# Performance work log

Hardware: AMD Instinct MI355X
Metric: run time of the kernel (lower is better)

Reference implementation:

```python
import jax, jax.numpy as jnp
import numpy as np

N_EMBD = 1024
N_HEADS = 16
HEAD_SIZE = N_EMBD // N_HEADS
B, T = 1, 4096
LN_EPS = 1e-5


def setup_inputs() -> dict:
    key = jax.random.key(0)
    ks = jax.random.split(key, 12)
    s = lambda fan_in: 1.0 / np.sqrt(fan_in)
    return {
        "x": jax.random.normal(ks[0], (B, T, N_EMBD), dtype=jnp.float32),
        # per-head Q/K/V projections (no bias), stacked over heads: [H, C, hd]
        "Wq": jax.random.normal(ks[1], (N_HEADS, N_EMBD, HEAD_SIZE), dtype=jnp.float32) * s(N_EMBD),
        "Wk": jax.random.normal(ks[2], (N_HEADS, N_EMBD, HEAD_SIZE), dtype=jnp.float32) * s(N_EMBD),
        "Wv": jax.random.normal(ks[3], (N_HEADS, N_EMBD, HEAD_SIZE), dtype=jnp.float32) * s(N_EMBD),
        # output projection (with bias)
        "Wp": jax.random.normal(ks[4], (N_EMBD, N_EMBD), dtype=jnp.float32) * s(N_EMBD),
        "bp": jnp.zeros((N_EMBD,), dtype=jnp.float32),
        # FFN: Linear(C, 4C) -> ReLU -> Linear(4C, C)
        "W1": jax.random.normal(ks[5], (N_EMBD, 4 * N_EMBD), dtype=jnp.float32) * s(N_EMBD),
        "b1": jnp.zeros((4 * N_EMBD,), dtype=jnp.float32),
        "W2": jax.random.normal(ks[6], (4 * N_EMBD, N_EMBD), dtype=jnp.float32) * s(4 * N_EMBD),
        "b2": jnp.zeros((N_EMBD,), dtype=jnp.float32),
        # LayerNorms
        "g1": jnp.ones((N_EMBD,), dtype=jnp.float32),
        "be1": jnp.zeros((N_EMBD,), dtype=jnp.float32),
        "g2": jnp.ones((N_EMBD,), dtype=jnp.float32),
        "be2": jnp.zeros((N_EMBD,), dtype=jnp.float32),
    }


def _layernorm(x, gamma, beta):
    mu = jnp.mean(x, axis=-1, keepdims=True)
    var = jnp.mean(jnp.square(x - mu), axis=-1, keepdims=True)
    return (x - mu) * jax.lax.rsqrt(var + LN_EPS) * gamma + beta


def _block(x, Wq, Wk, Wv, Wp, bp, W1, b1, W2, b2, g1, be1, g2, be2):
    Bn, Tn, C = x.shape
    h = _layernorm(x, g1, be1)
    # per-head projections: [B, H, T, hd]
    q = jnp.einsum("btc,hcd->bhtd", h, Wq)
    k = jnp.einsum("btc,hcd->bhtd", h, Wk)
    v = jnp.einsum("btc,hcd->bhtd", h, Wv)
    # NOTE: original scales by C**-0.5 where C = n_embd (not head_size)
    scores = jnp.einsum("bhtd,bhsd->bhts", q, k) * (C ** -0.5)
    causal = jnp.tril(jnp.ones((Tn, Tn), dtype=bool))
    scores = jnp.where(causal, scores, -jnp.inf)
    w = jax.nn.softmax(scores, axis=-1)
    attn = jnp.einsum("bhts,bhsd->bhtd", w, v)
    # concat heads: [B, T, H*hd] = [B, T, C]
    attn = attn.transpose(0, 2, 1, 3).reshape(Bn, Tn, C)
    x = x + attn @ Wp + bp
    h2 = _layernorm(x, g2, be2)
    ff = jax.nn.relu(h2 @ W1 + b1) @ W2 + b2
    return x + ff


def reference(x, Wq, Wk, Wv, Wp, bp, W1, b1, W2, b2, g1, be1, g2, be2):
    return _block(x, Wq, Wk, Wv, Wp, bp, W1, b1, W2, b2, g1, be1, g2, be2)
```

## Files before the change

kernel.cpp:

```cpp
#include <hip/hip_runtime.h>
#include <cstdint>

typedef __attribute__((ext_vector_type(8))) short bf16x8;
typedef __attribute__((ext_vector_type(4))) float f32x4;
typedef __attribute__((ext_vector_type(16))) float f32x16;
typedef __attribute__((ext_vector_type(4))) unsigned int u32x4;

__device__ __forceinline__ short f2b(float f) {
  unsigned u = __builtin_bit_cast(unsigned, f);
  unsigned r = (u + 0x7fffu + ((u >> 16) & 1u)) >> 16;
  return (short)(unsigned short)r;
}
__device__ __forceinline__ float b2f(short s) {
  unsigned u = ((unsigned)(unsigned short)s) << 16;
  return __builtin_bit_cast(float, u);
}

__device__ __forceinline__ void gload16(void* lds_dst, const void* gsrc) {
  __builtin_amdgcn_global_load_lds(
      (const __attribute__((address_space(1))) void*)gsrc,
      (__attribute__((address_space(3))) void*)lds_dst, 16, 0, 0);
}

__device__ __forceinline__ unsigned cvtpk(float a, float b) {
  unsigned r;
  asm("v_cvt_pk_bf16_f32 %0, %1, %2" : "=v"(r) : "v"(a), "v"(b));
  return r;
}
__device__ __forceinline__ unsigned shflx32(unsigned v) {
  return (unsigned)__shfl_xor((int)v, 32);
}
__device__ __forceinline__ float exp2x(float x) {
  float r;
  asm("v_exp_f32 %0, %1" : "=v"(r) : "v"(x));
  return r;
}

__device__ __forceinline__ void plswap(unsigned &a, unsigned &b) {
#if __has_builtin(__builtin_amdgcn_permlane32_swap)
  auto r = __builtin_amdgcn_permlane32_swap((int)a, (int)b, false, false);
  a = (unsigned)r[0];
  b = (unsigned)r[1];
#else
  const bool lo = ((threadIdx.x & 63) < 32);
  unsigned ax = shflx32(a), bx = shflx32(b);
  unsigned na = lo ? a : bx;
  unsigned nb = lo ? ax : b;
  a = na; b = nb;
#endif
}

__global__ __launch_bounds__(256)
void prep_all(const float* __restrict__ Wq, const float* __restrict__ Wk,
              const float* __restrict__ Wv, const float* __restrict__ Wp,
              const float* __restrict__ W1, const float* __restrict__ W2,
              const float* __restrict__ x, const float* __restrict__ g1,
              const float* __restrict__ be1,
              short* __restrict__ WqkvT, short* __restrict__ WpT,
              short* __restrict__ W1T, short* __restrict__ W2T,
              short* __restrict__ hbuf)
{
  const int id = blockIdx.x;
  if (id < 12288) {
    __shared__ float tl[32][33];
    const int tx = threadIdx.x & 31;
    const int ty = threadIdx.x >> 5;
    if (id < 3072) {
      const int which = id >> 10;
      const int rem = id & 1023;
      const int head = rem >> 6;
      const int tile = rem & 63;
      const int tc = tile >> 1, td = tile & 1;
      const float* src = (which == 0 ? Wq : which == 1 ? Wk : Wv) + (long)head * 65536;
#pragma unroll
      for (int i2 = 0; i2 < 4; ++i2) {
        int i = ty + i2 * 8;
        tl[i][tx] = src[(long)(tc * 32 + i) * 64 + td * 32 + tx];
      }
      __syncthreads();
      const long base = (long)which * 1024 + head * 64 + td * 32;
#pragma unroll
      for (int i2 = 0; i2 < 4; ++i2) {
        int i = ty + i2 * 8;
        WqkvT[(base + i) * 1024 + tc * 32 + tx] = f2b(tl[tx][i]);
      }
    } else {
      const float* src;
      short* dst;
      int rows, cols, bx, by;
      if (id < 4096) {
        src = Wp; dst = WpT; rows = 1024; cols = 1024;
        const int k = id - 3072; bx = k & 31; by = k >> 5;
      } else if (id < 8192) {
        src = W1; dst = W1T; rows = 1024; cols = 4096;
        const int k = id - 4096; bx = k & 127; by = k >> 7;
      } else {
        src = W2; dst = W2T; rows = 4096; cols = 1024;
        const int k = id - 8192; bx = k & 31; by = k >> 5;
      }
#pragma unroll
      for (int i2 = 0; i2 < 4; ++i2) {
        int i = ty + i2 * 8;
        tl[i][tx] = src[(long)(by * 32 + i) * cols + bx * 32 + tx];
      }
      __syncthreads();
#pragma unroll
      for (int i2 = 0; i2 < 4; ++i2) {
        int i = ty + i2 * 8;
        dst[(long)(bx * 32 + i) * rows + by * 32 + tx] = f2b(tl[tx][i]);
      }
    }
  } else {
    const int row = id - 12288;
    const int t = threadIdx.x;
    const float4 v = ((const float4*)(x + (long)row * 1024))[t];
    float s = v.x + v.y + v.z + v.w;
    float ss = v.x * v.x + v.y * v.y + v.z * v.z + v.w * v.w;
#pragma unroll
    for (int off = 1; off < 64; off <<= 1) {
      s += __shfl_xor(s, off);
      ss += __shfl_xor(ss, off);
    }
    __shared__ float red[8];
    const int wave = t >> 6, lane = t & 63;
    if (lane == 0) { red[wave] = s; red[4 + wave] = ss; }
    __syncthreads();
    s = red[0] + red[1] + red[2] + red[3];
    ss = red[4] + red[5] + red[6] + red[7];
    const float mu = s * (1.f / 1024.f);
    const float rstd = rsqrtf(ss * (1.f / 1024.f) - mu * mu + 1e-5f);
    const float4 gv = ((const float4*)g1)[t];
    const float4 bv = ((const float4*)be1)[t];
    short4 ov;
    ov.x = f2b((v.x - mu) * rstd * gv.x + bv.x);
    ov.y = f2b((v.y - mu) * rstd * gv.y + bv.y);
    ov.z = f2b((v.z - mu) * rstd * gv.z + bv.z);
    ov.w = f2b((v.w - mu) * rstd * gv.w + bv.w);
    *(short4*)(hbuf + (long)row * 1024 + t * 4) = ov;
  }
}

__global__ void vtrans(const short* __restrict__ qkv, short* __restrict__ Vt)
{
  __shared__ short tl[32][33];
  const int t0 = blockIdx.x * 32;
  const int c0 = blockIdx.y * 32;
  const int head = c0 >> 6, d0 = c0 & 63;
  const int tx = threadIdx.x;
#pragma unroll
  for (int i2 = 0; i2 < 4; ++i2) {
    int i = threadIdx.y + i2 * 8;
    tl[i][tx] = qkv[(long)(t0 + i) * 3072 + 2048 + c0 + tx];
  }
  __syncthreads();
#pragma unroll
  for (int i2 = 0; i2 < 4; ++i2) {
    int i = threadIdx.y + i2 * 8;
    Vt[(long)head * 262144 + (long)(d0 + i) * 4096 + t0 + tx] = tl[tx][i];
  }
}

__global__ __launch_bounds__(256)
void layernorm_bf16(const float* __restrict__ x, const float* __restrict__ g,
                    const float* __restrict__ be, short* __restrict__ outp)
{
  const int row = blockIdx.x;
  const int t = threadIdx.x;
  const float4 v = ((const float4*)(x + (long)row * 1024))[t];
  float s = v.x + v.y + v.z + v.w;
  float ss = v.x * v.x + v.y * v.y + v.z * v.z + v.w * v.w;
#pragma unroll
  for (int off = 1; off < 64; off <<= 1) {
    s += __shfl_xor(s, off);
    ss += __shfl_xor(ss, off);
  }
  __shared__ float red[8];
  const int wave = t >> 6, lane = t & 63;
  if (lane == 0) { red[wave] = s; red[4 + wave] = ss; }
  __syncthreads();
  s = red[0] + red[1] + red[2] + red[3];
  ss = red[4] + red[5] + red[6] + red[7];
  const float mu = s * (1.f / 1024.f);
  const float rstd = rsqrtf(ss * (1.f / 1024.f) - mu * mu + 1e-5f);
  const float4 gv = ((const float4*)g)[t];
  const float4 bv = ((const float4*)be)[t];
  short4 ov;
  ov.x = f2b((v.x - mu) * rstd * gv.x + bv.x);
  ov.y = f2b((v.y - mu) * rstd * gv.y + bv.y);
  ov.z = f2b((v.z - mu) * rstd * gv.z + bv.z);
  ov.w = f2b((v.w - mu) * rstd * gv.w + bv.w);
  *(short4*)(outp + (long)row * 1024 + t * 4) = ov;
}

template<int EPI>
__global__ __launch_bounds__(512, 2)
void gemm128(const short* __restrict__ A, const short* __restrict__ Bt,
             int N, int K, int NT,
             short* __restrict__ Cb, float* __restrict__ Cf,
             const float* __restrict__ bias, const float* __restrict__ resid)
{
  __shared__ __align__(16) short As[2 * 8192];
  __shared__ __align__(16) short Bs[2 * 8192];
  const int tid = threadIdx.x;
  const int lane = tid & 63;
  const int wave = tid >> 6;
  const int wm = wave >> 2;
  const int wn = wave & 3;
  const int l15 = lane & 15, lg = lane >> 4;

  const int nwg = gridDim.x * gridDim.y;
  const int lin = blockIdx.y * gridDim.x + blockIdx.x;
  const int swz = (lin & 7) * (nwg >> 3) + (lin >> 3);
  const long m0 = (long)(swz / gridDim.x) * 128;
  const long n0 = (long)(swz % gridDim.x) * 128;

  const int rloc = lane >> 3;
  const int csrc = (lane & 7) ^ rloc;
  const short* Ag = A + (m0 + wave * 8 + rloc) * K + csrc * 8;
  const short* Bg = Bt + (n0 + wave * 8 + rloc) * K + csrc * 8;
  const int wbase = wave * 512;

  f32x4 acc[4][2] = {};

#define STAGE128(buf, kt)                                                     \
  do {                                                                        \
    gload16(As + (buf) * 8192 + wbase, Ag + (kt));                            \
    gload16(As + (buf) * 8192 + 4096 + wbase, Ag + (long)64 * K + (kt));      \
    gload16(Bs + (buf) * 8192 + wbase, Bg + (kt));                            \
    gload16(Bs + (buf) * 8192 + 4096 + wbase, Bg + (long)64 * K + (kt));      \
  } while (0)

  STAGE128(0, 0);
  STAGE128(1, 64);
  asm volatile("s_waitcnt vmcnt(4)" ::: "memory");
  __builtin_amdgcn_sched_barrier(0);
  __builtin_amdgcn_s_barrier();
  __builtin_amdgcn_sched_barrier(0);

  const int cA = l15 & 7;
  for (int t = 0; t < NT; ++t) {
    const char* Ab = (const char*)(As + (t & 1) * 8192);
    const char* Bb = (const char*)(Bs + (t & 1) * 8192);
#pragma unroll
    for (int kk = 0; kk < 2; ++kk) {
      bf16x8 af[4], bk[2];
#pragma unroll
      for (int mi = 0; mi < 4; ++mi)
        af[mi] = *(const bf16x8*)(Ab + (wm * 64 + mi * 16 + l15) * 128 + 16 * ((kk * 4 + lg) ^ cA));
#pragma unroll
      for (int ni = 0; ni < 2; ++ni)
        bk[ni] = *(const bf16x8*)(Bb + (wn * 32 + ni * 16 + l15) * 128 + 16 * ((kk * 4 + lg) ^ cA));
      __builtin_amdgcn_s_setprio(1);
#pragma unroll
      for (int mi = 0; mi < 4; ++mi)
#pragma unroll
        for (int ni = 0; ni < 2; ++ni)
          acc[mi][ni] = __builtin_amdgcn_mfma_f32_16x16x32_bf16(af[mi], bk[ni], acc[mi][ni], 0, 0, 0);
      __builtin_amdgcn_s_setprio(0);
    }
    if (t == NT - 1) break;
    __builtin_amdgcn_s_barrier();
    __builtin_amdgcn_sched_barrier(0);
    if (t + 2 < NT) {
      STAGE128(t & 1, (long)(t + 2) * 64);
      asm volatile("s_waitcnt vmcnt(4)" ::: "memory");
    } else {
      asm volatile("s_waitcnt vmcnt(0)" ::: "memory");
    }
    __builtin_amdgcn_sched_barrier(0);
    __builtin_amdgcn_s_barrier();
    __builtin_amdgcn_sched_barrier(0);
  }
#undef STAGE128

#pragma unroll
  for (int mi = 0; mi < 4; ++mi) {
#pragma unroll
    for (int ni = 0; ni < 2; ++ni) {
      const long col = n0 + wn * 32 + ni * 16 + l15;
#pragma unroll
      for (int r = 0; r < 4; ++r) {
        const long row = m0 + wm * 64 + mi * 16 + lg * 4 + r;
        const long idx = row * N + col;
        float v = acc[mi][ni][r];
        if (EPI == 0) {
          Cb[idx] = f2b(v);
        } else {
          Cf[idx] = v + bias[col] + resid[idx];
        }
      }
    }
  }
}

__device__ __forceinline__ void stage256(short* AsB, short* BsB,
                                         const short* Ag, const short* Bg,
                                         long kt, int K, int ldsoff)
{
#pragma unroll
  for (int p = 0; p < 4; ++p)
    gload16(AsB + p * 4096 + ldsoff, Ag + (long)p * 64 * K + kt);
#pragma unroll
  for (int p = 0; p < 4; ++p)
    gload16(BsB + p * 4096 + ldsoff, Bg + (long)p * 64 * K + kt);
}

template<int EPI>
__global__ __launch_bounds__(512, 2)
void gemm256(const short* __restrict__ A, const short* __restrict__ Bt,
             int N, int K, int NT,
             short* __restrict__ Cb, const float* __restrict__ bias)
{
  __shared__ __align__(16) short As[2 * 16384];
  __shared__ __align__(16) short Bs[2 * 16384];
  const int tid = threadIdx.x;
  const int lane = tid & 63;
  const int wave = tid >> 6;
  const int wm = wave >> 2;
  const int wn = wave & 3;
  const int l15 = lane & 15, lg = lane >> 4;

  const int nwg = gridDim.x * gridDim.y;
  const int lin = blockIdx.y * gridDim.x + blockIdx.x;
  const int swz = (lin & 7) * (nwg >> 3) + (lin >> 3);
  const long m0 = (long)(swz / gridDim.x) * 256;
  const long n0 = (long)(swz % gridDim.x) * 256;

  const int trow = tid >> 3;
  const int csrc = (tid & 7) ^ (trow & 7);
  const short* Ag = A + (m0 + trow) * K + csrc * 8;
  const short* Bg = Bt + (n0 + trow) * K + csrc * 8;
  const int ldsoff = wave * 512;

  f32x4 acc[8][4] = {};

  stage256(As, Bs, Ag, Bg, 0, K, ldsoff);
  asm volatile("s_waitcnt vmcnt(0)" ::: "memory");
  __builtin_amdgcn_sched_barrier(0);
  __builtin_amdgcn_s_barrier();
  __builtin_amdgcn_sched_barrier(0);

  const int cA = l15 & 7;
  for (int t = 0; t < NT; ++t) {
    const char* Ab = (const char*)(As + (t & 1) * 16384);
    const char* Bb = (const char*)(Bs + (t & 1) * 16384);
    short* Asn = As + ((t + 1) & 1) * 16384;
    short* Bsn = Bs + ((t + 1) & 1) * 16384;
    const bool more = (t + 1 < NT);
    const long ktn = (long)(t + 1) * 64;
    bf16x8 bk[4];
#pragma unroll
    for (int ph = 0; ph < 4; ++ph) {
      const int kk = ph >> 1;
      const int mh = (ph & 1) * 4;
      bf16x8 af[4];
#pragma unroll
      for (int mi = 0; mi < 4; ++mi)
        af[mi] = *(const bf16x8*)(Ab + (wm * 128 + (mh + mi) * 16 + l15) * 128 + 16 * ((kk * 4 + lg) ^ cA));
      if ((ph & 1) == 0) {
#pragma unroll
        for (int ni = 0; ni < 4; ++ni)
          bk[ni] = *(const bf16x8*)(Bb + (wn * 64 + ni * 16 + l15) * 128 + 16 * ((kk * 4 + lg) ^ cA));
      }
      if (more && ph == 0) {
#pragma unroll
        for (int p = 0; p < 4; ++p)
          gload16(Asn + p * 4096 + ldsoff, Ag + (long)p * 64 * K + ktn);
      }
      if (more && ph == 1) {
#pragma unroll
        for (int p = 0; p < 4; ++p)
          gload16(Bsn + p * 4096 + ldsoff, Bg + (long)p * 64 * K + ktn);
      }
      __builtin_amdgcn_s_barrier();
      asm volatile("s_waitcnt lgkmcnt(0)" ::: "memory");
      __builtin_amdgcn_sched_barrier(0);
      __builtin_amdgcn_s_setprio(1);
#pragma unroll
      for (int mi = 0; mi < 4; ++mi)
#pragma unroll
        for (int ni = 0; ni < 4; ++ni)
          acc[mh + mi][ni] = __builtin_amdgcn_mfma_f32_16x16x32_bf16(af[mi], bk[ni], acc[mh + mi][ni], 0, 0, 0);
      __builtin_amdgcn_s_setprio(0);
      if (ph == 3 && more) {
        asm volatile("s_waitcnt vmcnt(0)" ::: "memory");
        __builtin_amdgcn_sched_barrier(0);
      }
      __builtin_amdgcn_s_barrier();
      __builtin_amdgcn_sched_barrier(0);
    }
  }

#pragma unroll
  for (int mi = 0; mi < 8; ++mi) {
#pragma unroll
    for (int ni = 0; ni < 4; ++ni) {
      const long col = n0 + wn * 64 + ni * 16 + l15;
      const float bb = (EPI == 2) ? bias[col] : 0.f;
#pragma unroll
      for (int r = 0; r < 4; ++r) {
        const long row = m0 + wm * 128 + mi * 16 + lg * 4 + r;
        float v = acc[mi][ni][r];
        if (EPI == 2) { v += bb; v = v > 0.f ? v : 0.f; }
        Cb[row * N + col] = f2b(v);
      }
    }
  }
}

__device__ __forceinline__ void stage_tile(short* lds, const short* gbase,
                                           long rstride, int wq, int lane)
{
  const int rloc = lane >> 3;
  const int chunk = (lane & 7) ^ rloc;
#pragma unroll
  for (int it = 0; it < 4; ++it) {
    const int row = wq * 32 + it * 8 + rloc;
    gload16(lds + (wq * 32 + it * 8) * 64, gbase + (long)row * rstride + chunk * 8);
  }
}

__global__ __launch_bounds__(256)
void attn_fwd3(const short* __restrict__ qkv, const short* __restrict__ Vt,
               short* __restrict__ outp)
{
  __shared__ __align__(16) short Ksm[4 * 4096];
  __shared__ __align__(16) short Vsm[4 * 4096];
  __shared__ __align__(16) short OB[64 * 64];
  __shared__ float lAll[128];

  const int tid = threadIdx.x;
  const int lane = tid & 63;
  const int wave = tid >> 6;
  const int pair = wave >> 1;
  const int wq = wave & 1;
  const int head = blockIdx.y;
  const int bx = blockIdx.x;
  const int l31 = lane & 31;
  const int h = lane >> 5;
  const int rs = l31 & 7;

  const short* Qg = qkv + head * 64;
  const short* Kg = qkv + 1024 + head * 64;
  const short* Vg = Vt + (long)head * 262144;

  for (int ph = 0; ph < 2; ++ph) {
    const int qsuper = ph ? (63 - bx) : bx;
    const int q0 = qsuper * 64 + wq * 32;
    const int q = q0 + l31;
    const int nt = qsuper + 1;
    const int ni = (nt + 1) >> 1;

    bf16x8 qf[4];
#pragma unroll
    for (int d = 0; d < 4; ++d) {
      bf16x8 tq = *(const bf16x8*)(Qg + (long)q * 3072 + d * 16 + h * 8);
#pragma unroll
      for (int j = 0; j < 8; ++j) tq[j] = f2b(b2f(tq[j]) * (0.03125f * 1.44269504f));
      qf[d] = tq;
    }

    float l_r = 0.f;
    f32x16 o0 = {}, o1 = {};

    if (pair < nt) {
      stage_tile(Ksm + pair * 4096, Kg + (long)(pair * 64) * 3072, 3072, wq, lane);
      stage_tile(Vsm + pair * 4096, Vg + pair * 64, 4096, wq, lane);
    }

    for (int ti = 0; ti < ni; ++ti) {
      const int t = 2 * ti + pair;
      const int tn = t + 2;
      if (ti > 0) {
        __builtin_amdgcn_s_barrier();
        __builtin_amdgcn_sched_barrier(0);
      }
      if (tn < nt) {
        stage_tile(Ksm + (tn & 3) * 4096, Kg + (long)(tn * 64) * 3072, 3072, wq, lane);
        stage_tile(Vsm + (tn & 3) * 4096, Vg + (long)(tn * 64), 4096, wq, lane);
        asm volatile("s_waitcnt vmcnt(8)" ::: "memory");
      } else {
        asm volatile("s_waitcnt vmcnt(0)" ::: "memory");
      }
      __builtin_amdgcn_sched_barrier(0);
      __builtin_amdgcn_s_barrier();
      __builtin_amdgcn_sched_barrier(0);
      if (t < nt) {
        const int kv0 = t * 64;
        const char* Kb = (const char*)(Ksm + (t & 3) * 4096);
        const char* Vb = (const char*)(Vsm + (t & 3) * 4096);
        f32x16 s0 = {}, s1 = {};
        __builtin_amdgcn_s_setprio(1);
#pragma unroll
        for (int d = 0; d < 4; ++d) {
          const int ck = ((d * 2 + h) ^ rs) * 16;
          const bf16x8 kf0 = *(const bf16x8*)(Kb + l31 * 128 + ck);
          const bf16x8 kf1 = *(const bf16x8*)(Kb + (32 + l31) * 128 + ck);
          s0 = __builtin_amdgcn_mfma_f32_32x32x16_bf16(kf0, qf[d], s0, 0, 0, 0);
          s1 = __builtin_amdgcn_mfma_f32_32x32x16_bf16(kf1, qf[d], s1, 0, 0, 0);
        }
        __builtin_amdgcn_s_setprio(0);
        if (t == qsuper) {
          const int kb = kv0 + 4 * h;
#pragma unroll
          for (int r = 0; r < 16; ++r) {
            const int k0 = kb + (r & 3) + 8 * (r >> 2);
            if (k0 > q) s0[r] = -INFINITY;
            if (k0 + 32 > q) s1[r] = -INFINITY;
          }
        }
#pragma unroll
        for (int r = 0; r < 16; ++r) {
          s0[r] = exp2x(s0[r]);
          s1[r] = exp2x(s1[r]);
        }
        {
          float sm[16];
#pragma unroll
          for (int r = 0; r < 16; ++r) sm[r] = s0[r] + s1[r];
#pragma unroll
          for (int st = 8; st >= 1; st >>= 1)
#pragma unroll
            for (int r = 0; r < 8; ++r)
              if (r < st) sm[r] += sm[r + st];
          l_r += sm[0] + __shfl_xor(sm[0], 32);
        }
        unsigned A0 = cvtpk(s0[0], s0[1]),   A1 = cvtpk(s0[2], s0[3]);
        unsigned A2 = cvtpk(s0[4], s0[5]),   A3 = cvtpk(s0[6], s0[7]);
        unsigned A4 = cvtpk(s0[8], s0[9]),   A5 = cvtpk(s0[10], s0[11]);
        unsigned A6 = cvtpk(s0[12], s0[13]), A7 = cvtpk(s0[14], s0[15]);
        unsigned B0 = cvtpk(s1[0], s1[1]),   B1 = cvtpk(s1[2], s1[3]);
        unsigned B2 = cvtpk(s1[4], s1[5]),   B3 = cvtpk(s1[6], s1[7]);
        unsigned B4 = cvtpk(s1[8], s1[9]),   B5 = cvtpk(s1[10], s1[11]);
        unsigned B6 = cvtpk(s1[12], s1[13]), B7 = cvtpk(s1[14], s1[15]);
        plswap(A0, A2); plswap(A1, A3); plswap(A4, A6); plswap(A5, A7);
        plswap(B0, B2); plswap(B1, B3); plswap(B4, B6); plswap(B5, B7);
        u32x4 fA0, fA1, fB0, fB1;
        fA0[0] = A0; fA0[1] = A1; fA0[2] = A2; fA0[3] = A3;
        fA1[0] = A4; fA1[1] = A5; fA1[2] = A6; fA1[3] = A7;
        fB0[0] = B0; fB0[1] = B1; fB0[2] = B2; fB0[3] = B3;
        fB1[0] = B4; fB1[1] = B5; fB1[2] = B6; fB1[3] = B7;
        const bf16x8 paA0 = __builtin_bit_cast(bf16x8, fA0);
        const bf16x8 paA1 = __builtin_bit_cast(bf16x8, fA1);
        const bf16x8 paB0 = __builtin_bit_cast(bf16x8, fB0);
        const bf16x8 paB1 = __builtin_bit_cast(bf16x8, fB1);
        __builtin_amdgcn_s_setprio(1);
        {
          const char* Vr0 = Vb + l31 * 128;
          const char* Vr1 = Vb + (32 + l31) * 128;
          const bf16x8 v00 = *(const bf16x8*)(Vr0 + ((0 + h) ^ rs) * 16);
          const bf16x8 v01 = *(const bf16x8*)(Vr0 + ((2 + h) ^ rs) * 16);
          const bf16x8 v02 = *(const bf16x8*)(Vr0 + ((4 + h) ^ rs) * 16);
          const bf16x8 v03 = *(const bf16x8*)(Vr0 + ((6 + h) ^ rs) * 16);
          o0 = __builtin_amdgcn_mfma_f32_32x32x16_bf16(paA0, v00, o0, 0, 0, 0);
          o0 = __builtin_amdgcn_mfma_f32_32x32x16_bf16(paA1, v01, o0, 0, 0, 0);
          o0 = __builtin_amdgcn_mfma_f32_32x32x16_bf16(paB0, v02, o0, 0, 0, 0);
          o0 = __builtin_amdgcn_mfma_f32_32x32x16_bf16(paB1, v03, o0, 0, 0, 0);
          const bf16x8 v10 = *(const bf16x8*)(Vr1 + ((0 + h) ^ rs) * 16);
          const bf16x8 v11 = *(const bf16x8*)(Vr1 + ((2 + h) ^ rs) * 16);
          const bf16x8 v12 = *(const bf16x8*)(Vr1 + ((4 + h) ^ rs) * 16);
          const bf16x8 v13 = *(const bf16x8*)(Vr1 + ((6 + h) ^ rs) * 16);
          o1 = __builtin_amdgcn_mfma_f32_32x32x16_bf16(paA0, v10, o1, 0, 0, 0);
          o1 = __builtin_amdgcn_mfma_f32_32x32x16_bf16(paA1, v11, o1, 0, 0, 0);
          o1 = __builtin_amdgcn_mfma_f32_32x32x16_bf16(paB0, v12, o1, 0, 0, 0);
          o1 = __builtin_amdgcn_mfma_f32_32x32x16_bf16(paB1, v13, o1, 0, 0, 0);
        }
        __builtin_amdgcn_s_setprio(0);
      }
    }

    lAll[wave * 32 + l31] = l_r;
    if (pair == 1) {
#pragma unroll
      for (int r = 0; r < 16; ++r) {
        const int qq = wq * 32 + (r & 3) + 8 * (r >> 2) + 4 * h;
        OB[qq * 64 + l31] = f2b(o0[r]);
        OB[qq * 64 + 32 + l31] = f2b(o1[r]);
      }
    }
    __syncthreads();
    if (pair == 0) {
#pragma unroll
      for (int r = 0; r < 16; ++r) {
        const int qo = (r & 3) + 8 * (r >> 2) + 4 * h;
        const int qq = wq * 32 + qo;
        const float lA = lAll[wq * 32 + qo];
        const float lB = lAll[64 + wq * 32 + qo];
        const float inv = 1.f / (lA + lB);
        const long qr = (long)qsuper * 64 + qq;
        const float v0 = o0[r] + b2f(OB[qq * 64 + l31]);
        const float v1 = o1[r] + b2f(OB[qq * 64 + 32 + l31]);
        outp[qr * 1024 + head * 64 + l31] = f2b(v0 * inv);
        outp[qr * 1024 + head * 64 + 32 + l31] = f2b(v1 * inv);
      }
    }
    __syncthreads();
  }
}

extern "C" void kernel_launch(void* const* d_in, const int* in_sizes, int n_in,
                              void* d_out, int out_size, void* d_ws, size_t ws_size,
                              hipStream_t stream)
{
  (void)in_sizes; (void)n_in; (void)out_size; (void)ws_size;
  const float* x   = (const float*)d_in[0];
  const float* Wq  = (const float*)d_in[1];
  const float* Wk  = (const float*)d_in[2];
  const float* Wv  = (const float*)d_in[3];
  const float* Wp  = (const float*)d_in[4];
  const float* bp  = (const float*)d_in[5];
  const float* W1  = (const float*)d_in[6];
  const float* b1  = (const float*)d_in[7];
  const float* W2  = (const float*)d_in[8];
  const float* b2  = (const float*)d_in[9];
  const float* g1  = (const float*)d_in[10];
  const float* be1 = (const float*)d_in[11];
  const float* g2  = (const float*)d_in[12];
  const float* be2 = (const float*)d_in[13];
  float* out = (float*)d_out;

  char* ws = (char*)d_ws;
  const size_t MB = 1ull << 20;
  short* WqkvT = (short*)(ws + 0 * MB);
  short* WpT   = (short*)(ws + 6 * MB);
  short* W1T   = (short*)(ws + 8 * MB);
  short* W2T   = (short*)(ws + 16 * MB);
  short* hbuf  = (short*)(ws + 24 * MB);
  short* qkvb  = (short*)(ws + 32 * MB);
  short* attnb = (short*)(ws + 56 * MB);
  float* x1    = (float*)(ws + 64 * MB);
  short* Vtb   = (short*)(ws + 64 * MB);

  prep_all<<<16384, 256, 0, stream>>>(Wq, Wk, Wv, Wp, W1, W2, x, g1, be1,
                                      WqkvT, WpT, W1T, W2T, hbuf);
  gemm256<0><<<dim3(12, 16), 512, 0, stream>>>(hbuf, WqkvT, 3072, 1024, 16,
                                               qkvb, nullptr);
  vtrans<<<dim3(128, 32), dim3(32, 8), 0, stream>>>(qkvb, Vtb);
  attn_fwd3<<<dim3(32, 16), 256, 0, stream>>>(qkvb, Vtb, attnb);
  gemm128<1><<<dim3(8, 32), 512, 0, stream>>>(attnb, WpT, 1024, 1024, 16,
                                              nullptr, x1, bp, x);
  layernorm_bf16<<<4096, 256, 0, stream>>>(x1, g2, be2, hbuf);
  gemm256<2><<<dim3(16, 16), 512, 0, stream>>>(hbuf, W1T, 4096, 1024, 16,
                                               qkvb, b1);
  gemm128<1><<<dim3(8, 32), 512, 0, stream>>>(qkvb, W2T, 1024, 4096, 64,
                                              nullptr, out, b2, x1);
}
```

Measured before the change: 269.0 us.

## Split attention KV work per wave with private LDS buffers and MFMA row sums

Restructures the attention kernel so each wave owns a private double-buffered LDS region and processes a 32-key half of every 64-key tile. This removes the block-wide barriers in the main loop. The softmax denominator is now accumulated with an MFMA against a ones vector instead of shuffle reductions. The 1D grid is also remapped so heads interleave across blocks. In exchange, K/V tiles are loaded separately per wave pair with a new V staging layout, and each block does more MFMA work for the row sums.

Measured after the change: 248.5 us. 1.08x faster.

```diff
diff --git a/kernel.cpp b/kernel.cpp
--- a/kernel.cpp
+++ b/kernel.cpp
@@ -408,48 +408,64 @@
   }
 }
 
-__device__ __forceinline__ void stage_tile(short* lds, const short* gbase,
-                                           long rstride, int wq, int lane)
-{
+__device__ __forceinline__ void stage_k32(short* lds, const short* gRowBase)
+{
+  const int lane = threadIdx.x & 63;
   const int rloc = lane >> 3;
-  const int chunk = (lane & 7) ^ rloc;
-#pragma unroll
-  for (int it = 0; it < 4; ++it) {
-    const int row = wq * 32 + it * 8 + rloc;
-    gload16(lds + (wq * 32 + it * 8) * 64, gbase + (long)row * rstride + chunk * 8);
+  const int cs = (lane & 7) ^ rloc;
+#pragma unroll
+  for (int p = 0; p < 4; ++p)
+    gload16(lds + p * 512, gRowBase + (long)(p * 8 + rloc) * 3072 + cs * 8);
+}
+__device__ __forceinline__ void stage_v32(short* lds, const short* vHeadBase, int t0)
+{
+  const int lane = threadIdx.x & 63;
+  const int rloc = lane >> 3;
+  const int cs = (lane & 7) ^ rloc;
+#pragma unroll
+  for (int p = 0; p < 4; ++p) {
+    const int row = p * 8 + rloc;
+    const int d = row + ((cs & 4) << 3);
+    gload16(lds + p * 512, vHeadBase + (long)d * 4096 + t0 + (cs & 3) * 8);
   }
 }
 
 __global__ __launch_bounds__(256)
-void attn_fwd3(const short* __restrict__ qkv, const short* __restrict__ Vt,
+void attn_fwd4(const short* __restrict__ qkv, const short* __restrict__ Vt,
                short* __restrict__ outp)
 {
-  __shared__ __align__(16) short Ksm[4 * 4096];
-  __shared__ __align__(16) short Vsm[4 * 4096];
+  __shared__ __align__(16) short KV[4 * 8192];
   __shared__ __align__(16) short OB[64 * 64];
-  __shared__ float lAll[128];
+  __shared__ float lAll[64];
 
   const int tid = threadIdx.x;
   const int lane = tid & 63;
   const int wave = tid >> 6;
-  const int pair = wave >> 1;
   const int wq = wave & 1;
-  const int head = blockIdx.y;
-  const int bx = blockIdx.x;
+  const int ks = wave >> 1;
   const int l31 = lane & 31;
   const int h = lane >> 5;
   const int rs = l31 & 7;
 
+  const int id = blockIdx.x;
+  const int head = ((id & 7) << 1) | (id >> 8);
+  const int bx = (id >> 3) & 31;
+
   const short* Qg = qkv + head * 64;
   const short* Kg = qkv + 1024 + head * 64;
   const short* Vg = Vt + (long)head * 262144;
+
+  short* Kw = KV + wave * 8192;
+
+  bf16x8 onesf;
+#pragma unroll
+  for (int j = 0; j < 8; ++j) onesf[j] = (short)0x3F80;
 
   for (int ph = 0; ph < 2; ++ph) {
     const int qsuper = ph ? (63 - bx) : bx;
     const int q0 = qsuper * 64 + wq * 32;
     const int q = q0 + l31;
     const int nt = qsuper + 1;
-    const int ni = (nt + 1) >> 1;
 
     bf16x8 qf[4];
 #pragma unroll
@@ -460,133 +476,96 @@
       qf[d] = tq;
     }
 
-    float l_r = 0.f;
-    f32x16 o0 = {}, o1 = {};
-
-    if (pair < nt) {
-      stage_tile(Ksm + pair * 4096, Kg + (long)(pair * 64) * 3072, 3072, wq, lane);
-      stage_tile(Vsm + pair * 4096, Vg + pair * 64, 4096, wq, lane);
-    }
-
-    for (int ti = 0; ti < ni; ++ti) {
-      const int t = 2 * ti + pair;
-      const int tn = t + 2;
-      if (ti > 0) {
-        __builtin_amdgcn_s_barrier();
-        __builtin_amdgcn_sched_barrier(0);
-      }
-      if (tn < nt) {
-        stage_tile(Ksm + (tn & 3) * 4096, Kg + (long)(tn * 64) * 3072, 3072, wq, lane);
-        stage_tile(Vsm + (tn & 3) * 4096, Vg + (long)(tn * 64), 4096, wq, lane);
+    f32x16 o0 = {}, o1 = {}, lacc = {};
+
+    stage_k32(Kw, Kg + (long)(ks * 32) * 3072);
+    stage_v32(Kw + 2048, Vg, ks * 32);
+    if (nt > 1) {
+      stage_k32(Kw + 4096, Kg + (long)(64 + ks * 32) * 3072);
+      stage_v32(Kw + 4096 + 2048, Vg, 64 + ks * 32);
+    }
+
+    for (int t = 0; t < nt; ++t) {
+      if (t + 1 < nt) {
         asm volatile("s_waitcnt vmcnt(8)" ::: "memory");
       } else {
         asm volatile("s_waitcnt vmcnt(0)" ::: "memory");
       }
       __builtin_amdgcn_sched_barrier(0);
-      __builtin_amdgcn_s_barrier();
+      const char* Kb = (const char*)(Kw + (t & 1) * 4096);
+      const char* Vb = Kb + 4096;
+      const bf16x8 kf0 = *(const bf16x8*)(Kb + l31 * 128 + 16 * ((0 + h) ^ rs));
+      const bf16x8 kf1 = *(const bf16x8*)(Kb + l31 * 128 + 16 * ((2 + h) ^ rs));
+      const bf16x8 kf2 = *(const bf16x8*)(Kb + l31 * 128 + 16 * ((4 + h) ^ rs));
+      const bf16x8 kf3 = *(const bf16x8*)(Kb + l31 * 128 + 16 * ((6 + h) ^ rs));
+      const bf16x8 vf00 = *(const bf16x8*)(Vb + l31 * 128 + 16 * ((0 + h) ^ rs));
+      const bf16x8 vf01 = *(const bf16x8*)(Vb + l31 * 128 + 16 * ((2 + h) ^ rs));
+      const bf16x8 vf10 = *(const bf16x8*)(Vb + l31 * 128 + 16 * ((4 + h) ^ rs));
+      const bf16x8 vf11 = *(const bf16x8*)(Vb + l31 * 128 + 16 * ((6 + h) ^ rs));
+      asm volatile("s_waitcnt lgkmcnt(0)" ::: "memory");
       __builtin_amdgcn_sched_barrier(0);
-      if (t < nt) {
-        const int kv0 = t * 64;
-        const char* Kb = (const char*)(Ksm + (t & 3) * 4096);
-        const char* Vb = (const char*)(Vsm + (t & 3) * 4096);
-        f32x16 s0 = {}, s1 = {};
-        __builtin_amdgcn_s_setprio(1);
-#pragma unroll
-        for (int d = 0; d < 4; ++d) {
-          const int ck = ((d * 2 + h) ^ rs) * 16;
-          const bf16x8 kf0 = *(const bf16x8*)(Kb + l31 * 128 + ck);
-          const bf16x8 kf1 = *(const bf16x8*)(Kb + (32 + l31) * 128 + ck);
-          s0 = __builtin_amdgcn_mfma_f32_32x32x16_bf16(kf0, qf[d], s0, 0, 0, 0);
-          s1 = __builtin_amdgcn_mfma_f32_32x32x16_bf16(kf1, qf[d], s1, 0, 0, 0);
+      if (t + 2 < nt) {
+        stage_k32(Kw + (t & 1) * 4096, Kg + (long)((t + 2) * 64 + ks * 32) * 3072);
+        stage_v32(Kw + (t & 1) * 4096 + 2048, Vg, (t + 2) * 64 + ks * 32);
+      }
+      f32x16 s = {};
+      __builtin_amdgcn_s_setprio(1);
+      s = __builtin_amdgcn_mfma_f32_32x32x16_bf16(kf0, qf[0], s, 0, 0, 0);
+      s = __builtin_amdgcn_mfma_f32_32x32x16_bf16(kf1, qf[1], s, 0, 0, 0);
+      s = __builtin_amdgcn_mfma_f32_32x32x16_bf16(kf2, qf[2], s, 0, 0, 0);
+      s = __builtin_amdgcn_mfma_f32_32x32x16_bf16(kf3, qf[3], s, 0, 0, 0);
+      __builtin_amdgcn_s_setprio(0);
+      if (t == qsuper) {
+        const int kb0 = t * 64 + ks * 32 + 4 * h;
+#pragma unroll
+        for (int r = 0; r < 16; ++r) {
+          const int k0 = kb0 + (r & 3) + 8 * (r >> 2);
+          if (k0 > q) s[r] = -INFINITY;
         }
-        __builtin_amdgcn_s_setprio(0);
-        if (t == qsuper) {
-          const int kb = kv0 + 4 * h;
-#pragma unroll
-          for (int r = 0; r < 16; ++r) {
-            const int k0 = kb + (r & 3) + 8 * (r >> 2);
-            if (k0 > q) s0[r] = -INFINITY;
-            if (k0 + 32 > q) s1[r] = -INFINITY;
-          }
-        }
-#pragma unroll
-        for (int r = 0; r < 16; ++r) {
-          s0[r] = exp2x(s0[r]);
-          s1[r] = exp2x(s1[r]);
-        }
-        {
-          float sm[16];
-#pragma unroll
-          for (int r = 0; r < 16; ++r) sm[r] = s0[r] + s1[r];
-#pragma unroll
-          for (int st = 8; st >= 1; st >>= 1)
-#pragma unroll
-            for (int r = 0; r < 8; ++r)
-              if (r < st) sm[r] += sm[r + st];
-          l_r += sm[0] + __shfl_xor(sm[0], 32);
-        }
-        unsigned A0 = cvtpk(s0[0], s0[1]),   A1 = cvtpk(s0[2], s0[3]);
-        unsigned A2 = cvtpk(s0[4], s0[5]),   A3 = cvtpk(s0[6], s0[7]);
-        unsigned A4 = cvtpk(s0[8], s0[9]),   A5 = cvtpk(s0[10], s0[11]);
-        unsigned A6 = cvtpk(s0[12], s0[13]), A7 = cvtpk(s0[14], s0[15]);
-        unsigned B0 = cvtpk(s1[0], s1[1]),   B1 = cvtpk(s1[2], s1[3]);
-        unsigned B2 = cvtpk(s1[4], s1[5]),   B3 = cvtpk(s1[6], s1[7]);
-        unsigned B4 = cvtpk(s1[8], s1[9]),   B5 = cvtpk(s1[10], s1[11]);
-        unsigned B6 = cvtpk(s1[12], s1[13]), B7 = cvtpk(s1[14], s1[15]);
-        plswap(A0, A2); plswap(A1, A3); plswap(A4, A6); plswap(A5, A7);
-        plswap(B0, B2); plswap(B1, B3); plswap(B4, B6); plswap(B5, B7);
-        u32x4 fA0, fA1, fB0, fB1;
-        fA0[0] = A0; fA0[1] = A1; fA0[2] = A2; fA0[3] = A3;
-        fA1[0] = A4; fA1[1] = A5; fA1[2] = A6; fA1[3] = A7;
-        fB0[0] = B0; fB0[1] = B1; fB0[2] = B2; fB0[3] = B3;
-        fB1[0] = B4; fB1[1] = B5; fB1[2] = B6; fB1[3] = B7;
-        const bf16x8 paA0 = __builtin_bit_cast(bf16x8, fA0);
-        const bf16x8 paA1 = __builtin_bit_cast(bf16x8, fA1);
-        const bf16x8 paB0 = __builtin_bit_cast(bf16x8, fB0);
-        const bf16x8 paB1 = __builtin_bit_cast(bf16x8, fB1);
-        __builtin_amdgcn_s_setprio(1);
-        {
-          const char* Vr0 = Vb + l31 * 128;
-          const char* Vr1 = Vb + (32 + l31) * 128;
-          const bf16x8 v00 = *(const bf16x8*)(Vr0 + ((0 + h) ^ rs) * 16);
-          const bf16x8 v01 = *(const bf16x8*)(Vr0 + ((2 + h) ^ rs) * 16);
-          const bf16x8 v02 = *(const bf16x8*)(Vr0 + ((4 + h) ^ rs) * 16);
-          const bf16x8 v03 = *(const bf16x8*)(Vr0 + ((6 + h) ^ rs) * 16);
-          o0 = __builtin_amdgcn_mfma_f32_32x32x16_bf16(paA0, v00, o0, 0, 0, 0);
-          o0 = __builtin_amdgcn_mfma_f32_32x32x16_bf16(paA1, v01, o0, 0, 0, 0);
-          o0 = __builtin_amdgcn_mfma_f32_32x32x16_bf16(paB0, v02, o0, 0, 0, 0);
-          o0 = __builtin_amdgcn_mfma_f32_32x32x16_bf16(paB1, v03, o0, 0, 0, 0);
-          const bf16x8 v10 = *(const bf16x8*)(Vr1 + ((0 + h) ^ rs) * 16);
-          const bf16x8 v11 = *(const bf16x8*)(Vr1 + ((2 + h) ^ rs) * 16);
-          const bf16x8 v12 = *(const bf16x8*)(Vr1 + ((4 + h) ^ rs) * 16);
-          const bf16x8 v13 = *(const bf16x8*)(Vr1 + ((6 + h) ^ rs) * 16);
-          o1 = __builtin_amdgcn_mfma_f32_32x32x16_bf16(paA0, v10, o1, 0, 0, 0);
-          o1 = __builtin_amdgcn_mfma_f32_32x32x16_bf16(paA1, v11, o1, 0, 0, 0);
-          o1 = __builtin_amdgcn_mfma_f32_32x32x16_bf16(paB0, v12, o1, 0, 0, 0);
-          o1 = __builtin_amdgcn_mfma_f32_32x32x16_bf16(paB1, v13, o1, 0, 0, 0);
-        }
-        __builtin_amdgcn_s_setprio(0);
-      }
-    }
-
-    lAll[wave * 32 + l31] = l_r;
-    if (pair == 1) {
+      }
+#pragma unroll
+      for (int r = 0; r < 16; ++r) s[r] = exp2x(s[r]);
+      unsigned P0 = cvtpk(s[0], s[1]),   P1 = cvtpk(s[2], s[3]);
+      unsigned P2 = cvtpk(s[4], s[5]),   P3 = cvtpk(s[6], s[7]);
+      unsigned P4 = cvtpk(s[8], s[9]),   P5 = cvtpk(s[10], s[11]);
+      unsigned P6 = cvtpk(s[12], s[13]), P7 = cvtpk(s[14], s[15]);
+      plswap(P0, P2); plswap(P1, P3); plswap(P4, P6); plswap(P5, P7);
+      u32x4 f0, f1;
+      f0[0] = P0; f0[1] = P1; f0[2] = P2; f0[3] = P3;
+      f1[0] = P4; f1[1] = P5; f1[2] = P6; f1[3] = P7;
+      const bf16x8 pa0 = __builtin_bit_cast(bf16x8, f0);
+      const bf16x8 pa1 = __builtin_bit_cast(bf16x8, f1);
+      __builtin_amdgcn_s_setprio(1);
+      o0 = __builtin_amdgcn_mfma_f32_32x32x16_bf16(pa0, vf00, o0, 0, 0, 0);
+      o0 = __builtin_amdgcn_mfma_f32_32x32x16_bf16(pa1, vf01, o0, 0, 0, 0);
+      o1 = __builtin_amdgcn_mfma_f32_32x32x16_bf16(pa0, vf10, o1, 0, 0, 0);
+      o1 = __builtin_amdgcn_mfma_f32_32x32x16_bf16(pa1, vf11, o1, 0, 0, 0);
+      lacc = __builtin_amdgcn_mfma_f32_32x32x16_bf16(pa0, onesf, lacc, 0, 0, 0);
+      lacc = __builtin_amdgcn_mfma_f32_32x32x16_bf16(pa1, onesf, lacc, 0, 0, 0);
+      __builtin_amdgcn_s_setprio(0);
+    }
+
+    if (ks == 1) {
 #pragma unroll
       for (int r = 0; r < 16; ++r) {
         const int qq = wq * 32 + (r & 3) + 8 * (r >> 2) + 4 * h;
         OB[qq * 64 + l31] = f2b(o0[r]);
         OB[qq * 64 + 32 + l31] = f2b(o1[r]);
       }
+      if (l31 == 0) {
+#pragma unroll
+        for (int r = 0; r < 16; ++r) {
+          const int qq = wq * 32 + (r & 3) + 8 * (r >> 2) + 4 * h;
+          lAll[qq] = lacc[r];
+        }
+      }
     }
     __syncthreads();
-    if (pair == 0) {
+    if (ks == 0) {
 #pragma unroll
       for (int r = 0; r < 16; ++r) {
-        const int qo = (r & 3) + 8 * (r >> 2) + 4 * h;
-        const int qq = wq * 32 + qo;
-        const float lA = lAll[wq * 32 + qo];
-        const float lB = lAll[64 + wq * 32 + qo];
-        const float inv = 1.f / (lA + lB);
+        const int qq = wq * 32 + (r & 3) + 8 * (r >> 2) + 4 * h;
+        const float inv = 1.f / (lacc[r] + lAll[qq]);
         const long qr = (long)qsuper * 64 + qq;
         const float v0 = o0[r] + b2f(OB[qq * 64 + l31]);
         const float v1 = o1[r] + b2f(OB[qq * 64 + 32 + l31]);
@@ -636,7 +615,7 @@
   gemm256<0><<<dim3(12, 16), 512, 0, stream>>>(hbuf, WqkvT, 3072, 1024, 16,
                                                qkvb, nullptr);
   vtrans<<<dim3(128, 32), dim3(32, 8), 0, stream>>>(qkvb, Vtb);
-  attn_fwd3<<<dim3(32, 16), 256, 0, stream>>>(qkvb, Vtb, attnb);
+  attn_fwd4<<<512, 256, 0, stream>>>(qkvb, Vtb, attnb);
   gemm128<1><<<dim3(8, 32), 512, 0, stream>>>(attnb, WpT, 1024, 1024, 16,
                                               nullptr, x1, bp, x);
   layernorm_bf16<<<4096, 256, 0, stream>>>(x1, g2, be2, hbuf);
```
